# Performance work log

Measured on AMD Instinct MI355X. Metric: run time of the kernel, lower is better.

Reference implementation:

```python
import jax, jax.numpy as jnp
import numpy as np

B, T, C, E, K = 4, 4096, 2048, 64, 8


def setup_inputs() -> dict:
    key = jax.random.key(0)
    k1, k2, k3 = jax.random.split(key, 3)
    hidden_states = jax.random.normal(k1, (B, T, C), dtype=jnp.float32)
    mask = jax.random.randint(k2, (B, T), 0, 2).astype(bool)
    gate_weight = jax.random.normal(k3, (E, C), dtype=jnp.float32) * 0.02
    gate_bias = jnp.zeros((E,), dtype=jnp.float32)
    expert_biases = jnp.zeros((E,), dtype=jnp.float32)
    return {
        "hidden_states": hidden_states,
        "mask": mask,
        "gate_weight": gate_weight,
        "gate_bias": gate_bias,
        "expert_biases": expert_biases,
    }


def reference(hidden_states, mask, gate_weight, gate_bias, expert_biases):
    Bc, Tc, Cc = hidden_states.shape
    n_experts = gate_weight.shape[0]
    x = hidden_states.reshape(-1, Cc)                 # [N, C]
    m = mask.reshape(-1)                              # [N]
    gate_output = x @ gate_weight.T + gate_bias       # [N, E]
    gate_probs = jax.nn.sigmoid(gate_output)
    gate_logits = gate_output + expert_biases
    _, top_k_indices = jax.lax.top_k(gate_logits, K)  # [N, K]
    top_k_probs = jnp.take_along_axis(gate_probs, top_k_indices, axis=-1)
    top_k_probs = top_k_probs / jnp.sum(top_k_probs, axis=-1, keepdims=True)
    # masked bincount of routed experts (only tokens where mask is True)
    weights = jnp.broadcast_to(m[:, None], top_k_indices.shape).astype(jnp.float32)
    expert_counts = jnp.zeros((n_experts,), jnp.float32).at[top_k_indices.reshape(-1)].add(weights.reshape(-1))
    avg_count = expert_counts.mean()
    maxvio = (expert_counts.max() - avg_count) / (avg_count + 1e-5)
    # note: the in-place expert_biases sign-update is a training-time, no-grad
    # side effect and does not change the returned values of this call.
    return top_k_indices, top_k_probs, maxvio
```

## Files before the change

### kernel.cpp

```cpp
#include <hip/hip_runtime.h>
#include <math.h>

#define NTOK   16384
#define CDIM   2048
#define NEXP   64
#define TOPK   8
#define KSPLIT 4

typedef _Float16 f16x8 __attribute__((ext_vector_type(8)));
typedef float    f32x4 __attribute__((ext_vector_type(4)));

__global__ __launch_bounds__(256) void pack_w16_kernel(
    const float* __restrict__ W,
    _Float16* __restrict__ Wh, _Float16* __restrict__ Wl)
{
    int t    = blockIdx.x * 256 + threadIdx.x;
    int lane = t & 63;
    int nt   = (t >> 6) & 3;
    int s    = t >> 8;
    int e    = nt * 16 + (lane & 15);
    int k    = s * 32 + (lane >> 4) * 8;
    const float* src = W + (size_t)e * CDIM + k;
    #pragma unroll
    for (int j = 0; j < 8; j++) {
        float x = src[j];
        _Float16 h = (_Float16)x;
        Wh[(size_t)t * 8 + j] = h;
        Wl[(size_t)t * 8 + j] = (_Float16)(x - (float)h);
    }
}

__global__ __launch_bounds__(256, 4) void gemm_f16split_kernel(
    const float* __restrict__ x,
    const _Float16* __restrict__ Wh,
    const _Float16* __restrict__ Wl,
    float* __restrict__ part)
{
    const int lane = threadIdx.x & 63;
    const int wid  = threadIdx.x >> 6;
    const int tb   = blockIdx.x & 255;
    const int pp   = blockIdx.x >> 8;
    const int tok0 = tb * 64 + wid * 16;
    const int q    = lane >> 4;
    const size_t xbase = (size_t)(tok0 + (lane & 15)) * CDIM + pp * 512 + q * 8;

    f32x4 acc[4];
    #pragma unroll
    for (int nt = 0; nt < 4; nt++) acc[nt] = (f32x4){0.f, 0.f, 0.f, 0.f};

    for (int s = 0; s < 16; s++) {
        const int S = pp * 16 + s;
        float4 v0 = *(const float4*)&x[xbase + s * 32];
        float4 v1 = *(const float4*)&x[xbase + s * 32 + 4];
        float xr[8] = {v0.x, v0.y, v0.z, v0.w, v1.x, v1.y, v1.z, v1.w};
        f16x8 ah, al;
        #pragma unroll
        for (int j = 0; j < 8; j++) {
            _Float16 h = (_Float16)xr[j];
            ah[j] = h;
            al[j] = (_Float16)(xr[j] - (float)h);
        }
        const f16x8* bhp = (const f16x8*)(Wh + ((size_t)S * 4 * 64 + lane) * 8);
        const f16x8* blp = (const f16x8*)(Wl + ((size_t)S * 4 * 64 + lane) * 8);
        #pragma unroll
        for (int nt = 0; nt < 4; nt++) {
            f16x8 bh = bhp[nt * 64];
            f16x8 bl = blp[nt * 64];
            acc[nt] = __builtin_amdgcn_mfma_f32_16x16x32_f16(ah, bh, acc[nt], 0, 0, 0);
            acc[nt] = __builtin_amdgcn_mfma_f32_16x16x32_f16(al, bh, acc[nt], 0, 0, 0);
            acc[nt] = __builtin_amdgcn_mfma_f32_16x16x32_f16(ah, bl, acc[nt], 0, 0, 0);
        }
    }

    #pragma unroll
    for (int nt = 0; nt < 4; nt++) {
        #pragma unroll
        for (int r = 0; r < 4; r++) {
            size_t tok = (size_t)tok0 + q * 4 + r;
            part[((size_t)pp * NTOK + tok) * NEXP + nt * 16 + (lane & 15)] = acc[nt][r];
        }
    }
}

__global__ __launch_bounds__(64) void reduce_topk_kernel(
    const float* __restrict__ part,
    const int*   __restrict__ mask,
    const float* __restrict__ gbias,
    const float* __restrict__ ebias,
    float*       __restrict__ out,
    float*       __restrict__ blockcnt)
{
    __shared__ unsigned int cnt[NEXP];
    const int lane = threadIdx.x;
    const int t = blockIdx.x * 64 + lane;
    cnt[lane] = 0u;
    __syncthreads();

    float z[NEXP];
    #pragma unroll
    for (int c = 0; c < 16; c++) {
        float4 v = *(const float4*)&part[(size_t)t * NEXP + c * 4];
        z[c*4+0] = v.x; z[c*4+1] = v.y; z[c*4+2] = v.z; z[c*4+3] = v.w;
    }
    #pragma unroll
    for (int p = 1; p < KSPLIT; p++) {
        #pragma unroll
        for (int c = 0; c < 16; c++) {
            float4 v = *(const float4*)&part[((size_t)p * NTOK + t) * NEXP + c * 4];
            z[c*4+0] += v.x; z[c*4+1] += v.y; z[c*4+2] += v.z; z[c*4+3] += v.w;
        }
    }
    float eb[NEXP];
    #pragma unroll
    for (int e = 0; e < NEXP; e++) {
        z[e] += gbias[e];
        eb[e] = ebias[e];
    }

    unsigned long long used = 0ull;
    int idxs[TOPK]; float probs[TOPK]; float psum = 0.f;
    #pragma unroll
    for (int r = 0; r < TOPK; r++) {
        float bv = -INFINITY, bz = 0.f; int bi = 0;
        #pragma unroll
        for (int e = 0; e < NEXP; e++) {
            float v = ((used >> e) & 1ull) ? -INFINITY : (z[e] + eb[e]);
            if (v > bv) { bv = v; bz = z[e]; bi = e; }
        }
        used |= 1ull << bi;
        idxs[r] = bi;
        float p = 1.f / (1.f + expf(-bz));
        probs[r] = p; psum += p;
    }
    float inv = 1.f / psum;

    float4 i0 = {(float)idxs[0], (float)idxs[1], (float)idxs[2], (float)idxs[3]};
    float4 i1 = {(float)idxs[4], (float)idxs[5], (float)idxs[6], (float)idxs[7]};
    float4 p0 = {probs[0]*inv, probs[1]*inv, probs[2]*inv, probs[3]*inv};
    float4 p1 = {probs[4]*inv, probs[5]*inv, probs[6]*inv, probs[7]*inv};
    *(float4*)&out[(size_t)t * TOPK + 0] = i0;
    *(float4*)&out[(size_t)t * TOPK + 4] = i1;
    *(float4*)&out[(size_t)NTOK * TOPK + (size_t)t * TOPK + 0] = p0;
    *(float4*)&out[(size_t)NTOK * TOPK + (size_t)t * TOPK + 4] = p1;

    if (mask[t] != 0) {
        #pragma unroll
        for (int r = 0; r < TOPK; r++) atomicAdd(&cnt[idxs[r]], 1u);
    }
    __syncthreads();
    blockcnt[(size_t)blockIdx.x * NEXP + lane] = (float)cnt[lane];
}

__global__ __launch_bounds__(256) void finalize_kernel(
    const float* __restrict__ blockcnt, float* __restrict__ out)
{
    __shared__ float ps[4][NEXP];
    const int t = threadIdx.x;
    const int e = t & 63, c = t >> 6;
    float s = 0.f;
    #pragma unroll 8
    for (int b = 0; b < 64; b++)
        s += blockcnt[(size_t)(c * 64 + b) * NEXP + e];
    ps[c][e] = s;
    __syncthreads();
    if (t < 64) {
        float tot = ps[0][t] + ps[1][t] + ps[2][t] + ps[3][t];
        float mx = tot, sm = tot;
        #pragma unroll
        for (int o = 32; o > 0; o >>= 1) {
            mx = fmaxf(mx, __shfl_down(mx, o));
            sm += __shfl_down(sm, o);
        }
        if (t == 0) {
            float avg = sm / (float)NEXP;
            out[2 * NTOK * TOPK] = (mx - avg) / (avg + 1e-5f);
        }
    }
}

__global__ __launch_bounds__(256) void fused_fallback_kernel(
    const float* __restrict__ x, const int* __restrict__ mask,
    const float* __restrict__ W, const float* __restrict__ gbias,
    const float* __restrict__ ebias, float* __restrict__ out,
    unsigned int* __restrict__ counts)
{
    __shared__ float As[64][36];
    __shared__ float Bs[64][36];
    __shared__ float Lg[64][NEXP + 1];
    __shared__ float s_gb[NEXP], s_eb[NEXP];
    __shared__ unsigned int s_cnt[NEXP];
    const int tid = threadIdx.x;
    const int tx = tid & 15, ty = tid >> 4;
    const int m0 = blockIdx.x * 64;
    if (tid < NEXP) { s_gb[tid] = gbias[tid]; s_eb[tid] = ebias[tid]; s_cnt[tid] = 0u; }
    float acc[4][4] = {};
    for (int kb = 0; kb < CDIM; kb += 32) {
        __syncthreads();
        #pragma unroll
        for (int p = 0; p < 2; p++) {
            int lin = tid + p * 256; int m = lin >> 3; int c4 = (lin & 7) << 2;
            *(float4*)&As[m][c4] = *(const float4*)&x[(size_t)(m0 + m) * CDIM + kb + c4];
            *(float4*)&Bs[m][c4] = *(const float4*)&W[(size_t)m * CDIM + kb + c4];
        }
        __syncthreads();
        #pragma unroll
        for (int k4 = 0; k4 < 32; k4 += 4) {
            float4 a[4], b[4];
            #pragma unroll
            for (int i = 0; i < 4; i++) a[i] = *(const float4*)&As[ty * 4 + i][k4];
            #pragma unroll
            for (int j = 0; j < 4; j++) b[j] = *(const float4*)&Bs[tx * 4 + j][k4];
            #pragma unroll
            for (int i = 0; i < 4; i++)
                #pragma unroll
                for (int j = 0; j < 4; j++)
                    acc[i][j] += a[i].x * b[j].x + a[i].y * b[j].y
                               + a[i].z * b[j].z + a[i].w * b[j].w;
        }
    }
    __syncthreads();
    #pragma unroll
    for (int i = 0; i < 4; i++)
        #pragma unroll
        for (int j = 0; j < 4; j++)
            Lg[ty * 4 + i][tx * 4 + j] = acc[i][j] + s_gb[tx * 4 + j];
    __syncthreads();
    if (tid < 64) {
        const int g = m0 + tid;
        unsigned long long used = 0ull;
        int idxs[TOPK]; float probs[TOPK]; float psum = 0.f;
        #pragma unroll
        for (int k = 0; k < TOPK; k++) {
            float best = -INFINITY; int bi = 0;
            for (int n = 0; n < NEXP; n++) {
                if ((used >> n) & 1ull) continue;
                float vv = Lg[tid][n] + s_eb[n];
                if (vv > best) { best = vv; bi = n; }
            }
            used |= (1ull << bi);
            idxs[k] = bi;
            float p = 1.f / (1.f + expf(-Lg[tid][bi]));
            probs[k] = p; psum += p;
        }
        float inv = 1.f / psum;
        #pragma unroll
        for (int k = 0; k < TOPK; k++) {
            out[(size_t)g * TOPK + k] = (float)idxs[k];
            out[(size_t)NTOK * TOPK + (size_t)g * TOPK + k] = probs[k] * inv;
        }
        if (mask[g] != 0)
            #pragma unroll
            for (int k = 0; k < TOPK; k++) atomicAdd(&s_cnt[idxs[k]], 1u);
    }
    __syncthreads();
    if (tid < NEXP && s_cnt[tid] != 0u) atomicAdd(&counts[tid], s_cnt[tid]);
}

__global__ void finalize_atomic_kernel(const unsigned int* __restrict__ counts,
                                       float* __restrict__ out)
{
    const int t = threadIdx.x;
    float c  = (float)counts[t];
    float mx = c, sm = c;
    #pragma unroll
    for (int o = 32; o > 0; o >>= 1) {
        mx = fmaxf(mx, __shfl_down(mx, o));
        sm += __shfl_down(sm, o);
    }
    if (t == 0) {
        float avg = sm / (float)NEXP;
        out[2 * NTOK * TOPK] = (mx - avg) / (avg + 1e-5f);
    }
}

extern "C" void kernel_launch(void* const* d_in, const int* in_sizes, int n_in,
                              void* d_out, int out_size, void* d_ws, size_t ws_size,
                              hipStream_t stream)
{
    const float* x     = (const float*)d_in[0];
    const int*   mask  = (const int*)  d_in[1];
    const float* W     = (const float*)d_in[2];
    const float* gbias = (const float*)d_in[3];
    const float* ebias = (const float*)d_in[4];
    float* out = (float*)d_out;

    const size_t whB  = (size_t)NEXP * CDIM * sizeof(_Float16);
    const size_t bcB  = (size_t)256 * NEXP * sizeof(float);
    const size_t ptB  = (size_t)KSPLIT * NTOK * NEXP * sizeof(float);
    const size_t need = 2 * whB + bcB + ptB;

    if (ws_size >= need) {
        _Float16* Wh = (_Float16*)d_ws;
        _Float16* Wl = (_Float16*)((char*)d_ws + whB);
        float* blockcnt = (float*)((char*)d_ws + 2 * whB);
        float* part = (float*)((char*)d_ws + 2 * whB + bcB);

        pack_w16_kernel<<<64, 256, 0, stream>>>(W, Wh, Wl);
        gemm_f16split_kernel<<<256 * KSPLIT, 256, 0, stream>>>(x, Wh, Wl, part);
        reduce_topk_kernel<<<256, 64, 0, stream>>>(part, mask, gbias, ebias, out, blockcnt);
        finalize_kernel<<<1, 256, 0, stream>>>(blockcnt, out);
        return;
    }

    unsigned int* counts = (unsigned int*)d_ws;
    hipMemsetAsync(d_ws, 0, NEXP * sizeof(unsigned int), stream);
    fused_fallback_kernel<<<NTOK / 64, 256, 0, stream>>>(x, mask, W, gbias, ebias, out, counts);
    finalize_atomic_kernel<<<1, 64, 0, stream>>>(counts, out);
}
```

Before: 231.0 us.

## Parallelize per-token top-k across 16 lanes with shuffle-based argmax

The reduce/top-k kernel previously used one thread per token, holding 64 logits in registers and scanning serially, with only 256 blocks of 64 threads. It now gives each token 16 lanes, each owning 4 experts. Each of the 8 top-k rounds uses an xor-shuffle argmax with lowest-index tie-breaking. Loads become coalesced float4 per lane, the grid grows to 1024 blocks of 256 threads, and finalize and the workspace are resized to match. The aim is to cut register pressure and serial work and to raise occupancy, at the cost of more shuffles and a larger per-block count buffer.

Result: no change. 233.2 us (+0.9%).

```diff
diff --git a/kernel.cpp b/kernel.cpp
--- a/kernel.cpp
+++ b/kernel.cpp
@@ -6,6 +6,7 @@
 #define NEXP   64
 #define TOPK   8
 #define KSPLIT 4
+#define RBLK   1024
 
 typedef _Float16 f16x8 __attribute__((ext_vector_type(8)));
 typedef float    f32x4 __attribute__((ext_vector_type(4)));
@@ -82,7 +83,7 @@
     }
 }
 
-__global__ __launch_bounds__(64) void reduce_topk_kernel(
+__global__ __launch_bounds__(256) void reduce_topk_kernel(
     const float* __restrict__ part,
     const int*   __restrict__ mask,
     const float* __restrict__ gbias,
@@ -91,64 +92,58 @@
     float*       __restrict__ blockcnt)
 {
     __shared__ unsigned int cnt[NEXP];
-    const int lane = threadIdx.x;
-    const int t = blockIdx.x * 64 + lane;
-    cnt[lane] = 0u;
-    __syncthreads();
-
-    float z[NEXP];
-    #pragma unroll
-    for (int c = 0; c < 16; c++) {
-        float4 v = *(const float4*)&part[(size_t)t * NEXP + c * 4];
-        z[c*4+0] = v.x; z[c*4+1] = v.y; z[c*4+2] = v.z; z[c*4+3] = v.w;
-    }
-    #pragma unroll
-    for (int p = 1; p < KSPLIT; p++) {
-        #pragma unroll
-        for (int c = 0; c < 16; c++) {
-            float4 v = *(const float4*)&part[((size_t)p * NTOK + t) * NEXP + c * 4];
-            z[c*4+0] += v.x; z[c*4+1] += v.y; z[c*4+2] += v.z; z[c*4+3] += v.w;
-        }
-    }
-    float eb[NEXP];
-    #pragma unroll
-    for (int e = 0; e < NEXP; e++) {
-        z[e] += gbias[e];
-        eb[e] = ebias[e];
-    }
-
-    unsigned long long used = 0ull;
-    int idxs[TOPK]; float probs[TOPK]; float psum = 0.f;
+    const int tid = threadIdx.x;
+    if (tid < NEXP) cnt[tid] = 0u;
+    __syncthreads();
+
+    const int t = blockIdx.x * 16 + (tid >> 4);
+    const int l = tid & 15;
+
+    float4 v = make_float4(0.f, 0.f, 0.f, 0.f);
+    #pragma unroll
+    for (int p = 0; p < KSPLIT; p++) {
+        float4 u = *(const float4*)&part[((size_t)p * NTOK + t) * NEXP + l * 4];
+        v.x += u.x; v.y += u.y; v.z += u.z; v.w += u.w;
+    }
+    float4 gb = *(const float4*)&gbias[l * 4];
+    float4 eb = *(const float4*)&ebias[l * 4];
+    float z[4], sel[4];
+    z[0] = v.x + gb.x; z[1] = v.y + gb.y; z[2] = v.z + gb.z; z[3] = v.w + gb.w;
+    sel[0] = z[0] + eb.x; sel[1] = z[1] + eb.y;
+    sel[2] = z[2] + eb.z; sel[3] = z[3] + eb.w;
+
+    int   idxs[TOPK];
+    float probs[TOPK];
+    float psum = 0.f;
+
     #pragma unroll
     for (int r = 0; r < TOPK; r++) {
-        float bv = -INFINITY, bz = 0.f; int bi = 0;
-        #pragma unroll
-        for (int e = 0; e < NEXP; e++) {
-            float v = ((used >> e) & 1ull) ? -INFINITY : (z[e] + eb[e]);
-            if (v > bv) { bv = v; bz = z[e]; bi = e; }
-        }
-        used |= 1ull << bi;
-        idxs[r] = bi;
+        float bv = -INFINITY, bz = 0.f; int bidx = 1 << 30;
+        #pragma unroll
+        for (int i = 0; i < 4; i++)
+            if (sel[i] > bv) { bv = sel[i]; bz = z[i]; bidx = l * 4 + i; }
+        #pragma unroll
+        for (int m = 1; m < 16; m <<= 1) {
+            float ov = __shfl_xor(bv, m);
+            float oz = __shfl_xor(bz, m);
+            int   oi = __shfl_xor(bidx, m);
+            if (ov > bv || (ov == bv && oi < bidx)) { bv = ov; bz = oz; bidx = oi; }
+        }
+        idxs[r] = bidx;
         float p = 1.f / (1.f + expf(-bz));
         probs[r] = p; psum += p;
-    }
+        if ((bidx >> 2) == l) sel[bidx & 3] = -INFINITY;
+    }
+
     float inv = 1.f / psum;
-
-    float4 i0 = {(float)idxs[0], (float)idxs[1], (float)idxs[2], (float)idxs[3]};
-    float4 i1 = {(float)idxs[4], (float)idxs[5], (float)idxs[6], (float)idxs[7]};
-    float4 p0 = {probs[0]*inv, probs[1]*inv, probs[2]*inv, probs[3]*inv};
-    float4 p1 = {probs[4]*inv, probs[5]*inv, probs[6]*inv, probs[7]*inv};
-    *(float4*)&out[(size_t)t * TOPK + 0] = i0;
-    *(float4*)&out[(size_t)t * TOPK + 4] = i1;
-    *(float4*)&out[(size_t)NTOK * TOPK + (size_t)t * TOPK + 0] = p0;
-    *(float4*)&out[(size_t)NTOK * TOPK + (size_t)t * TOPK + 4] = p1;
-
-    if (mask[t] != 0) {
-        #pragma unroll
-        for (int r = 0; r < TOPK; r++) atomicAdd(&cnt[idxs[r]], 1u);
-    }
-    __syncthreads();
-    blockcnt[(size_t)blockIdx.x * NEXP + lane] = (float)cnt[lane];
+    if (l < TOPK) {
+        out[(size_t)t * TOPK + l] = (float)idxs[l];
+        out[(size_t)NTOK * TOPK + (size_t)t * TOPK + l] = probs[l] * inv;
+        if (mask[t] != 0) atomicAdd(&cnt[idxs[l]], 1u);
+    }
+    __syncthreads();
+    if (tid < NEXP)
+        blockcnt[(size_t)blockIdx.x * NEXP + tid] = (float)cnt[tid];
 }
 
 __global__ __launch_bounds__(256) void finalize_kernel(
@@ -159,8 +154,8 @@
     const int e = t & 63, c = t >> 6;
     float s = 0.f;
     #pragma unroll 8
-    for (int b = 0; b < 64; b++)
-        s += blockcnt[(size_t)(c * 64 + b) * NEXP + e];
+    for (int b = 0; b < RBLK / 4; b++)
+        s += blockcnt[(size_t)(c * (RBLK / 4) + b) * NEXP + e];
     ps[c][e] = s;
     __syncthreads();
     if (t < 64) {
@@ -285,7 +280,7 @@
     float* out = (float*)d_out;
 
     const size_t whB  = (size_t)NEXP * CDIM * sizeof(_Float16);
-    const size_t bcB  = (size_t)256 * NEXP * sizeof(float);
+    const size_t bcB  = (size_t)RBLK * NEXP * sizeof(float);
     const size_t ptB  = (size_t)KSPLIT * NTOK * NEXP * sizeof(float);
     const size_t need = 2 * whB + bcB + ptB;
 
@@ -297,7 +292,7 @@
 
         pack_w16_kernel<<<64, 256, 0, stream>>>(W, Wh, Wl);
         gemm_f16split_kernel<<<256 * KSPLIT, 256, 0, stream>>>(x, Wh, Wl, part);
-        reduce_topk_kernel<<<256, 64, 0, stream>>>(part, mask, gbias, ebias, out, blockcnt);
+        reduce_topk_kernel<<<RBLK, 256, 0, stream>>>(part, mask, gbias, ebias, out, blockcnt);
         finalize_kernel<<<1, 256, 0, stream>>>(blockcnt, out);
         return;
     }
```
